# Kernel tuning notes

Measured on AMD Instinct MI355X. Metric: run time of the kernel, lower is better.

Reference implementation:

```python
import jax, jax.numpy as jnp
import numpy as np

TEMPERATURE = 1.0
CHUNK = 128  # node-block size for the curvature pass


def setup_inputs() -> dict:
    key = jax.random.key(0)
    k1, k2 = jax.random.split(key)
    N, D = 4096, 64
    x = jax.random.normal(k1, (N, D), dtype=jnp.float32)
    # sparse binary adjacency (avg degree ~16) + ring so min degree >= 2
    A = (jax.random.uniform(k2, (N, N)) < 0.004).astype(jnp.float32)
    i = jnp.arange(N)
    A = A.at[i, i].set(0.0)
    A = A.at[i, (i + 1) % N].set(1.0)
    A = A.at[(i + 1) % N, i].set(1.0)
    return {"node_embeddings": x, "adj_matrix": A}


def _physics_components(x, A):
    N, d = x.shape
    mask = A > 0
    deg = jnp.sum(A, axis=-1)                      # [N]

    # ---- total energy ----
    kinetic = jnp.sum(x * x, axis=-1)
    nb = A @ x                                     # neighbor aggregate [N,d]
    potential = -jnp.sum(x * nb, axis=-1)
    total_energy = kinetic + potential / (deg + 1e-8)

    # ---- local entropy over neighbor similarities ----
    xn = x / jnp.maximum(jnp.linalg.norm(x, axis=-1, keepdims=True), 1e-12)
    S = xn @ xn.T                                  # cosine sims [N,N]
    logits = jnp.where(mask, S / TEMPERATURE, -1e30)
    P = jax.nn.softmax(logits, axis=-1)            # masked softmax per row
    local_entropy = -jnp.sum(jnp.where(mask, P * jnp.log(P + 1e-8), 0.0), axis=-1)

    # ---- equilibrium deviation (5-NN local mean in embedding space) ----
    sq = jnp.sum(x * x, axis=-1)
    D2 = jnp.maximum(sq[:, None] + sq[None, :] - 2.0 * (x @ x.T), 1e-12)
    dist = jnp.sqrt(D2)                            # [N,N]
    _, idx = jax.lax.top_k(-dist, 6)               # smallest 6 (self first)
    local_means = jnp.mean(x[idx[:, 1:]], axis=1)  # [N,d]
    gdev = jnp.linalg.norm(x - jnp.mean(x, axis=0, keepdims=True), axis=-1)
    ldev = jnp.linalg.norm(x - local_means, axis=-1)
    equilibrium_deviation = 0.6 * gdev + 0.4 * ldev

    # ---- structural centrality ----
    en = jnp.linalg.norm(x, axis=-1)
    structural_centrality = 0.5 * deg / (N - 1) + 0.5 * en / jnp.max(en)

    # ---- information flow: unbiased var of neighbor sims ----
    ms = jnp.sum(jnp.where(mask, S, 0.0), axis=-1) / deg
    information_flow = jnp.sum(jnp.where(mask, (S - ms[:, None]) ** 2, 0.0), axis=-1) / (deg - 1.0)

    # ---- stability: 1/(1 + mean unbiased var of neighbor embeddings) ----
    m1 = nb / deg[:, None]
    ex2 = A @ (x * x)
    var_dim = (ex2 - deg[:, None] * m1 * m1) / (deg - 1.0)[:, None]
    stability = 1.0 / (1.0 + jnp.mean(var_dim, axis=-1))

    # ---- discrete curvature: 1 - mean pairwise cos angle of centered neighbors ----
    # mean_{j<k} u_j.u_k = (||sum u||^2 - sum ||u||^2) / (deg*(deg-1))
    def body(_, ids):
        xb = x[ids]                                 # [B,d]
        mb = mask[ids]                              # [B,N]
        c = x[None, :, :] - xb[:, None, :]          # [B,N,d]
        nrm = jnp.sqrt(jnp.maximum(jnp.sum(c * c, -1), 1e-12))
        u = jnp.where(mb[..., None], c / jnp.maximum(nrm, 1e-8)[..., None], 0.0)
        s = jnp.sum(u, axis=1)                      # [B,d]
        ssq = jnp.sum(u * u, axis=(1, 2))           # [B]
        db = jnp.sum(mb.astype(x.dtype), axis=-1)
        mean_cos = (jnp.sum(s * s, -1) - ssq) / (db * (db - 1.0))
        return None, 1.0 - mean_cos

    _, curv = jax.lax.scan(body, None, jnp.arange(N).reshape(-1, CHUNK))
    graph_curvature = curv.reshape(N)

    return (total_energy, local_entropy, equilibrium_deviation,
            structural_centrality, information_flow, stability, graph_curvature)


def reference(node_embeddings, adj_matrix):
    return _physics_components(node_embeddings, adj_matrix)
```

## Files before the change

### kernel.cpp

```cpp
#include <hip/hip_runtime.h>
#include <math.h>

#define NN 4096
#define DD 64
#define NSPLIT 64
#define JW 64

typedef _Float16 half8 __attribute__((ext_vector_type(8)));
typedef float f32x4 __attribute__((ext_vector_type(4)));

__device__ __forceinline__ unsigned sxu(unsigned v, int o){
  return (unsigned)__shfl_xor((int)v, o, 64);
}
__device__ __forceinline__ unsigned umn(unsigned a, unsigned b){ return a<b?a:b; }
__device__ __forceinline__ unsigned umx(unsigned a, unsigned b){ return a<b?b:a; }

__device__ __forceinline__ unsigned packkey32(float m, int j){
  float q = fmaf(m, 2048.f, 524288.f);
  q = fminf(fmaxf(q, 0.f), 1048575.f);
  return (((unsigned)q) << 12) | (unsigned)j;
}

__device__ __forceinline__ void ins5u(unsigned k, unsigned b[5]){
  bool c0=k<b[0], c1=k<b[1], c2=k<b[2], c3=k<b[3], c4=k<b[4];
  b[4] = c3 ? b[3] : (c4 ? k : b[4]);
  b[3] = c2 ? b[2] : (c3 ? k : b[3]);
  b[2] = c1 ? b[1] : (c2 ? k : b[2]);
  b[1] = c0 ? b[0] : (c1 ? k : b[1]);
  b[0] = c0 ? k : b[0];
}

__device__ __forceinline__ void mergeStage32(unsigned b[5], int st){
  unsigned p0=sxu(b[0],st),p1=sxu(b[1],st),p2=sxu(b[2],st),p3=sxu(b[3],st),p4=sxu(b[4],st);
  unsigned o0=umn(b[0],p0);
  unsigned o1=umn(umn(b[1],p1), umx(b[0],p0));
  unsigned o2=umn(umn(b[2],p2), umn(umx(b[0],p1),umx(b[1],p0)));
  unsigned o3=umn(umn(b[3],p3), umn(umx(b[0],p2), umn(umx(b[1],p1),umx(b[2],p0))));
  unsigned o4=umn(umn(b[4],p4), umn(umn(umx(b[0],p3),umx(b[1],p2)),
                                    umn(umx(b[2],p1),umx(b[3],p0))));
  b[0]=o0;b[1]=o1;b[2]=o2;b[3]=o3;b[4]=o4;
}

__device__ __forceinline__ void mergeLocal32(const unsigned a[5], const unsigned c[5], unsigned b[5]){
  b[0]=umn(a[0],c[0]);
  b[1]=umn(umn(a[1],c[1]), umx(a[0],c[0]));
  b[2]=umn(umn(a[2],c[2]), umn(umx(a[0],c[1]),umx(a[1],c[0])));
  b[3]=umn(umn(a[3],c[3]), umn(umx(a[0],c[2]), umn(umx(a[1],c[1]),umx(a[2],c[0]))));
  b[4]=umn(umn(a[4],c[4]), umn(umn(umx(a[0],c[3]),umx(a[1],c[2])),
                               umn(umx(a[2],c[1]),umx(a[3],c[0]))));
}

__global__ __launch_bounds__(256) void k_prec(const float* __restrict__ x,
                      float* __restrict__ sq,
                      _Float16* __restrict__ xh, _Float16* __restrict__ xl,
                      float* __restrict__ msum_part, float* __restrict__ maxsq_part){
  __shared__ float part[4][64];
  __shared__ float mxp[4];
  const int w = threadIdx.x>>6, lane = threadIdx.x&63;
  const int n0 = blockIdx.x*16 + w*4;
  float v0 = x[(size_t)(n0+0)*DD + lane];
  float v1 = x[(size_t)(n0+1)*DD + lane];
  float v2 = x[(size_t)(n0+2)*DD + lane];
  float v3 = x[(size_t)(n0+3)*DD + lane];
  float s0=v0*v0, s1=v1*v1, s2=v2*v2, s3=v3*v3;
#pragma unroll
  for(int o=1;o<64;o<<=1){
    s0 += __shfl_xor(s0,o,64); s1 += __shfl_xor(s1,o,64);
    s2 += __shfl_xor(s2,o,64); s3 += __shfl_xor(s3,o,64);
  }
  float vv[4] = {v0,v1,v2,v3};
  float ss[4] = {s0,s1,s2,s3};
#pragma unroll
  for(int q=0;q<4;q++){
    float v = vv[q];
    _Float16 h = (_Float16)v;
    _Float16 l = (_Float16)(v - (float)h);
    xh[(size_t)(n0+q)*DD+lane] = h;
    xl[(size_t)(n0+q)*DD+lane] = l;
    if(lane==0) sq[n0+q]=ss[q];
  }
  if(lane==0) mxp[w] = fmaxf(fmaxf(s0,s1), fmaxf(s2,s3));
  part[w][lane] = v0+v1+v2+v3; __syncthreads();
  if(w==0){
    msum_part[blockIdx.x*64 + lane] = part[0][lane]+part[1][lane]+part[2][lane]+part[3][lane];
    if(lane==0) maxsq_part[blockIdx.x] = fmaxf(fmaxf(mxp[0],mxp[1]), fmaxf(mxp[2],mxp[3]));
  }
}

__device__ __forceinline__ f32x4 gram6(const half8 J[4],
    half8 Ih0, half8 Ih1, half8 Il0, half8 Il1){
  const f32x4 z = {0.f,0.f,0.f,0.f};
  f32x4 a1 = __builtin_amdgcn_mfma_f32_16x16x32_f16(J[0], Ih0, z, 0,0,0);
  f32x4 a2 = __builtin_amdgcn_mfma_f32_16x16x32_f16(J[2], Ih0, z, 0,0,0);
  a1 = __builtin_amdgcn_mfma_f32_16x16x32_f16(J[1], Ih1, a1, 0,0,0);
  a2 = __builtin_amdgcn_mfma_f32_16x16x32_f16(J[3], Ih1, a2, 0,0,0);
  a1 = __builtin_amdgcn_mfma_f32_16x16x32_f16(J[0], Il0, a1, 0,0,0);
  a1 = __builtin_amdgcn_mfma_f32_16x16x32_f16(J[1], Il1, a1, 0,0,0);
  return a1 + a2;
}

__global__ __launch_bounds__(256, 4) void k_mega(
    const float* __restrict__ x, const float* __restrict__ A,
    const float* __restrict__ sq,
    const _Float16* __restrict__ xh, const _Float16* __restrict__ xl,
    unsigned* __restrict__ cand,
    const float* __restrict__ msum_part, const float* __restrict__ maxsq_part,
    float* __restrict__ msum, float* __restrict__ max_sq, float* __restrict__ deg_out,
    float* __restrict__ o_te, float* __restrict__ o_ent,
    float* __restrict__ o_if, float* __restrict__ o_st, float* __restrict__ o_cv)
{
  __shared__ int   nbr[4][128];
  __shared__ float Sval[4][128];
  __shared__ float rr[4][64];
  __shared__ float rm[4];
  __shared__ _Float16 jHi[512*8];
  __shared__ _Float16 jLo[512*8];
  const int bid = blockIdx.x;
  const int tid = threadIdx.x;
  const int w = tid>>6, lane = tid&63;

  if(bid == 0){
    float s = 0.f;
    for(int p=w; p<256; p+=4) s += msum_part[p*64 + lane];
    rr[w][lane] = s;
    float m = maxsq_part[w*64 + lane];
#pragma unroll
    for(int o=1;o<64;o<<=1) m = fmaxf(m, __shfl_xor(m,o,64));
    if(lane==0) rm[w] = m;
    __syncthreads();
    if(w==0){
      msum[lane] = rr[0][lane]+rr[1][lane]+rr[2][lane]+rr[3][lane];
      if(lane==0) max_sq[0] = fmaxf(fmaxf(rm[0],rm[1]), fmaxf(rm[2],rm[3]));
    }
    return;
  }

  const int t = bid - 1;
  if(t % 5 == 0){
    const int i = (t/5)*4 + w;
    const float xid = x[(size_t)i*DD + lane];
    const float sqi = sq[i];
    const float eni = sqrtf(sqi);
    const float4* A4 = (const float4*)(A + (size_t)i*NN);

    int deg = 0;
    for(int ch=0; ch<4; ++ch){
      float4 av[4];
#pragma unroll
      for(int qq=0; qq<4; ++qq) av[qq] = A4[lane + 64*(ch*4+qq)];
      int c = 0;
#pragma unroll
      for(int qq=0; qq<4; ++qq)
        c += (av[qq].x>0.f)+(av[qq].y>0.f)+(av[qq].z>0.f)+(av[qq].w>0.f);
      int sc = c;
#pragma unroll
      for(int o=1;o<64;o<<=1){ int v=__shfl_up(sc,o,64); if(lane>=o) sc+=v; }
      int off = deg + sc - c;
#pragma unroll
      for(int qq=0; qq<4; ++qq){
        int jb = 4*(lane + 64*(ch*4+qq));
        if(av[qq].x>0.f){ if(off<128) nbr[w][off]=jb+0; off++; }
        if(av[qq].y>0.f){ if(off<128) nbr[w][off]=jb+1; off++; }
        if(av[qq].z>0.f){ if(off<128) nbr[w][off]=jb+2; off++; }
        if(av[qq].w>0.f){ if(off<128) nbr[w][off]=jb+3; off++; }
      }
      deg += __shfl(sc, 63, 64);
    }

    const float degf = (float)deg;
    const int dmax = min(deg, 128);
    float nb_d=0.f, ex2_d=0.f, s_d=0.f, ssq=0.f;

    for(int c0=0; c0<dmax; c0+=8){
      int jq[8]; float aq[8], qq[8];
#pragma unroll
      for(int q=0;q<8;q++) jq[q] = nbr[w][min(c0+q, dmax-1)];
#pragma unroll
      for(int q=0;q<8;q++) aq[q] = x[(size_t)jq[q]*DD + lane];
#pragma unroll
      for(int q=0;q<8;q++) qq[q] = sq[jq[q]];
      asm volatile("" :: "v"(aq[0]), "v"(aq[1]), "v"(aq[2]), "v"(aq[3]),
                         "v"(aq[4]), "v"(aq[5]), "v"(aq[6]), "v"(aq[7]));
      float p[8];
#pragma unroll
      for(int q=0;q<8;q++) p[q] = xid*aq[q];
#pragma unroll
      for(int o=1;o<64;o<<=1){
#pragma unroll
        for(int q=0;q<8;q++) p[q] += __shfl_xor(p[q],o,64);
      }
#pragma unroll
      for(int q=0;q<8;q++){
        const bool valid = (c0+q) < deg;
        float c2 = fmaxf(sqi + qq[q] - 2.0f*p[q], 1e-12f);
        float inv = 1.0f/fmaxf(sqrtf(c2), 1e-8f);
        nb_d  += valid ? aq[q] : 0.f;
        ex2_d += valid ? aq[q]*aq[q] : 0.f;
        s_d   += valid ? (aq[q]-xid)*inv : 0.f;
        ssq   += valid ? c2*inv*inv : 0.f;
        if(valid && lane==q) Sval[w][c0+q] = p[q]/(eni*sqrtf(qq[q]));
      }
    }

    float t0 = xid*nb_d;
    float m1 = nb_d/degf;
    float t1 = (ex2_d - degf*m1*m1)/(degf-1.0f);
    float t2 = s_d*s_d;
    float t3 = 0.f, t4 = 0.f;
    for(int s=lane; s<dmax; s+=64){ float v=Sval[w][s]; t3 += expf(v); t4 += v; }
#pragma unroll
    for(int o=1;o<64;o<<=1){
      t0 += __shfl_xor(t0,o,64); t1 += __shfl_xor(t1,o,64); t2 += __shfl_xor(t2,o,64);
      t3 += __shfl_xor(t3,o,64); t4 += __shfl_xor(t4,o,64);
    }
    const float pot = t0, varm = t1*(1.0f/DD), s2 = t2, se = t3, ms = t4/degf;

    float e0=0.f, e1=0.f;
    const float inv_se = 1.0f/se;
    for(int s=lane; s<dmax; s+=64){
      float v = Sval[w][s];
      float pp = expf(v)*inv_se;
      e0 -= pp*logf(pp + 1e-8f);
      float dv = v-ms; e1 += dv*dv;
    }
#pragma unroll
    for(int o=1;o<64;o<<=1){ e0 += __shfl_xor(e0,o,64); e1 += __shfl_xor(e1,o,64); }

    if(lane==0){
      o_te[i]  = sqi - pot/(degf + 1e-8f);
      o_ent[i] = e0;
      o_if[i]  = e1/(degf-1.0f);
      o_st[i]  = 1.0f/(1.0f + varm);
      o_cv[i]  = 1.0f - (s2 - ssq)/(degf*(degf-1.0f));
      deg_out[i] = degf;
    }
  } else {
    const int kid = (t/5)*4 + (t%5) - 1;
    const int split = kid & (NSPLIT-1);
    const int strip = (kid >> 6)*4 + w;
    const int ibase = strip*16, j0 = split*JW;
    const int col = lane & 15, kg = lane >> 4;
    const int vo = col*DD + kg*8;
    const int myi = ibase + col;

#pragma unroll
    for(int q=0;q<2;q++){
      int g = q*256 + tid;
      int r = g >> 3;
      int c = (g & 7) ^ (r & 7);
      const _Float16* srcH = xh + (size_t)(j0 + r)*DD + c*8;
      const _Float16* srcL = xl + (size_t)(j0 + r)*DD + c*8;
      __builtin_amdgcn_global_load_lds(
        (const __attribute__((address_space(1))) unsigned int*)srcH,
        (__attribute__((address_space(3))) unsigned int*)(jHi + g*8), 16, 0, 0);
      __builtin_amdgcn_global_load_lds(
        (const __attribute__((address_space(1))) unsigned int*)srcL,
        (__attribute__((address_space(3))) unsigned int*)(jLo + g*8), 16, 0, 0);
    }

    const _Float16* pih = xh + (size_t)ibase*DD + vo;
    const _Float16* pil = xl + (size_t)ibase*DD + vo;
    const half8 Ih0 = *(const half8*)(pih);
    const half8 Ih1 = *(const half8*)(pih+32);
    const half8 Il0 = *(const half8*)(pil);
    const half8 Il1 = *(const half8*)(pil+32);

    const int jb0 = j0 + kg*4;
    float4 sq0 = *(const float4*)(sq + jb0);
    float4 sq1 = *(const float4*)(sq + jb0 + 16);
    float4 sq2 = *(const float4*)(sq + jb0 + 32);
    float4 sq3 = *(const float4*)(sq + jb0 + 48);

    __syncthreads();

    half8 JT[4][4];
#pragma unroll
    for(int tt=0; tt<4; tt++){
      const int rl = tt*16 + col;
      const int sw = rl & 7;
      JT[tt][0] = *(const half8*)(jHi + (rl*8 + ( kg      ^ sw))*8);
      JT[tt][1] = *(const half8*)(jHi + (rl*8 + ((kg + 4) ^ sw))*8);
      JT[tt][2] = *(const half8*)(jLo + (rl*8 + ( kg      ^ sw))*8);
      JT[tt][3] = *(const half8*)(jLo + (rl*8 + ((kg + 4) ^ sw))*8);
    }

    f32x4 d0 = gram6(JT[0], Ih0, Ih1, Il0, Il1);
    f32x4 d1 = gram6(JT[1], Ih0, Ih1, Il0, Il1);
    f32x4 d2 = gram6(JT[2], Ih0, Ih1, Il0, Il1);
    f32x4 d3 = gram6(JT[3], Ih0, Ih1, Il0, Il1);

    unsigned bA[5], bB[5];
#pragma unroll
    for(int k=0;k<5;k++){ bA[k]=0xFFFFFFFFu; bB[k]=0xFFFFFFFFu; }

    {
      float s0v[4]={sq0.x,sq0.y,sq0.z,sq0.w};
      float s2v[4]={sq2.x,sq2.y,sq2.z,sq2.w};
#pragma unroll
      for(int r=0;r<4;r++){
        unsigned k0 = packkey32(fmaf(-2.0f, d0[r], s0v[r]), jb0+r);
        k0 = (jb0+r==myi) ? 0xFFFFFFFFu : k0;
        ins5u(k0, bA);
        unsigned k2 = packkey32(fmaf(-2.0f, d2[r], s2v[r]), jb0+32+r);
        k2 = (jb0+32+r==myi) ? 0xFFFFFFFFu : k2;
        ins5u(k2, bA);
      }
    }
    {
      float s1v[4]={sq1.x,sq1.y,sq1.z,sq1.w};
      float s3v[4]={sq3.x,sq3.y,sq3.z,sq3.w};
#pragma unroll
      for(int r=0;r<4;r++){
        unsigned k1 = packkey32(fmaf(-2.0f, d1[r], s1v[r]), jb0+16+r);
        k1 = (jb0+16+r==myi) ? 0xFFFFFFFFu : k1;
        ins5u(k1, bB);
        unsigned k3 = packkey32(fmaf(-2.0f, d3[r], s3v[r]), jb0+48+r);
        k3 = (jb0+48+r==myi) ? 0xFFFFFFFFu : k3;
        ins5u(k3, bB);
      }
    }

    unsigned b[5];
    mergeLocal32(bA, bB, b);
    mergeStage32(b, 16);
    mergeStage32(b, 32);

    if(kg==0){
#pragma unroll
      for(int k=0;k<5;k++)
        cand[((size_t)myi*NSPLIT + split)*5 + k] = b[k];
    }
  }
}

__global__ __launch_bounds__(256) void k_nnsel(
    const float* __restrict__ x, const unsigned* __restrict__ cand,
    const float* __restrict__ msum, const float* __restrict__ max_sq,
    const float* __restrict__ deg, const float* __restrict__ sq,
    float* __restrict__ o_eq, float* __restrict__ o_sc)
{
  const int w = threadIdx.x>>6, l = threadIdx.x&63;
  const int i = blockIdx.x*4 + w;
  const unsigned* cr = cand + (size_t)i*(NSPLIT*5);
  unsigned c0 = cr[l], c1 = cr[64+l], c2 = cr[128+l], c3 = cr[192+l], c4 = cr[256+l];

  int sel[5];
#pragma unroll
  for(int k=0;k<5;k++){
    unsigned d = umn(umn(umn(c0,c1),umn(c2,c3)),c4);
#pragma unroll
    for(int o=1;o<64;o<<=1) d = umn(d, sxu(d,o));
    sel[k] = (int)(d & 0xFFFu);
    if(c0==d) c0=0xFFFFFFFFu;
    else if(c1==d) c1=0xFFFFFFFFu;
    else if(c2==d) c2=0xFFFFFFFFu;
    else if(c3==d) c3=0xFFFFFFFFu;
    else if(c4==d) c4=0xFFFFFFFFu;
  }

  float smv=0.f;
#pragma unroll
  for(int k=0;k<5;k++) smv += x[(size_t)sel[k]*DD + l];
  float xiv = x[(size_t)i*DD + l];
  float lv = xiv - smv*0.2f;
  float gv = xiv - msum[l]*(1.0f/NN);
  float pl = lv*lv, pg = gv*gv;
#pragma unroll
  for(int o=1;o<64;o<<=1){ pl += __shfl_xor(pl,o,64); pg += __shfl_xor(pg,o,64); }
  if(l==0){
    o_eq[i] = 0.6f*sqrtf(pg) + 0.4f*sqrtf(pl);
    o_sc[i] = 0.5f*deg[i]/(float)(NN-1) + 0.5f*sqrtf(sq[i])/sqrtf(max_sq[0]);
  }
}

extern "C" void kernel_launch(void* const* d_in, const int* in_sizes, int n_in,
                              void* d_out, int out_size, void* d_ws, size_t ws_size,
                              hipStream_t stream) {
  const float* x = (const float*)d_in[0];
  const float* A = (const float*)d_in[1];
  float* out = (float*)d_out;
  float* ws  = (float*)d_ws;
  float*     sq        = ws;
  float*     msum      = ws + 4096;
  float*     max_sq    = ws + 4160;
  float*     deg       = ws + 4224;
  float*     msum_part = ws + 8320;
  float*     maxsq_part= ws + 24704;
  _Float16*  xh        = (_Float16*)(ws + 24960);
  _Float16*  xl        = (_Float16*)(ws + 156032);
  unsigned*  cand      = (unsigned*)(ws + 287104);

  k_prec<<<NN/16, 256, 0, stream>>>(x, sq, xh, xl, msum_part, maxsq_part);
  k_mega<<<5*NN/4 + 1, 256, 0, stream>>>(x, A, sq, xh, xl, cand,
                                         msum_part, maxsq_part, msum, max_sq, deg,
                                         out, out+NN, out+4*NN, out+5*NN, out+6*NN);
  k_nnsel<<<NN/4, 256, 0, stream>>>(x, cand, msum, max_sq, deg, sq,
                                    out+2*NN, out+3*NN);
}
```

Baseline: 58.81 us.

## Widen KNN column tiles to 256 with double-buffered LDS staging, fewer splits

Each KNN block now covers 256 candidate columns in four 64-column chunks instead of one chunk. It double-buffers the fp16 hi/lo tiles in LDS so the next chunk's async global-to-LDS load overlaps the current chunk's MFMA and top-5 insertion. With 16 splits instead of 64, the grid interleaves row-stat blocks and KNN blocks 1:1 and writes a quarter as many candidates, which simplifies the final selection merge. The cost is fewer, longer blocks, twice the LDS tile footprint, and a sync per chunk.

```diff
diff --git a/kernel.cpp b/kernel.cpp
--- a/kernel.cpp
+++ b/kernel.cpp
@@ -3,8 +3,8 @@
 
 #define NN 4096
 #define DD 64
-#define NSPLIT 64
-#define JW 64
+#define NSPLIT 16
+#define JW 256
 
 typedef _Float16 half8 __attribute__((ext_vector_type(8)));
 typedef float f32x4 __attribute__((ext_vector_type(4)));
@@ -113,8 +113,8 @@
   __shared__ float Sval[4][128];
   __shared__ float rr[4][64];
   __shared__ float rm[4];
-  __shared__ _Float16 jHi[512*8];
-  __shared__ _Float16 jLo[512*8];
+  __shared__ _Float16 jHi[2][512*8];
+  __shared__ _Float16 jLo[2][512*8];
   const int bid = blockIdx.x;
   const int tid = threadIdx.x;
   const int w = tid>>6, lane = tid&63;
@@ -136,8 +136,8 @@
   }
 
   const int t = bid - 1;
-  if(t % 5 == 0){
-    const int i = (t/5)*4 + w;
+  if((t & 1) == 0){
+    const int i = (t>>1)*4 + w;
     const float xid = x[(size_t)i*DD + lane];
     const float sqi = sq[i];
     const float eni = sqrtf(sqi);
@@ -235,28 +235,31 @@
       deg_out[i] = degf;
     }
   } else {
-    const int kid = (t/5)*4 + (t%5) - 1;
+    const int kid = t >> 1;
     const int split = kid & (NSPLIT-1);
-    const int strip = (kid >> 6)*4 + w;
+    const int strip = (kid >> 4)*4 + w;
     const int ibase = strip*16, j0 = split*JW;
     const int col = lane & 15, kg = lane >> 4;
     const int vo = col*DD + kg*8;
     const int myi = ibase + col;
 
-#pragma unroll
-    for(int q=0;q<2;q++){
-      int g = q*256 + tid;
-      int r = g >> 3;
-      int c = (g & 7) ^ (r & 7);
-      const _Float16* srcH = xh + (size_t)(j0 + r)*DD + c*8;
-      const _Float16* srcL = xl + (size_t)(j0 + r)*DD + c*8;
-      __builtin_amdgcn_global_load_lds(
-        (const __attribute__((address_space(1))) unsigned int*)srcH,
-        (__attribute__((address_space(3))) unsigned int*)(jHi + g*8), 16, 0, 0);
-      __builtin_amdgcn_global_load_lds(
-        (const __attribute__((address_space(1))) unsigned int*)srcL,
-        (__attribute__((address_space(3))) unsigned int*)(jLo + g*8), 16, 0, 0);
-    }
+#define STAGE(BUF, CH) { \
+    _Pragma("unroll") \
+    for(int q_=0;q_<2;q_++){ \
+      int g_ = q_*256 + tid; \
+      int r_ = g_ >> 3; \
+      int c_ = (g_ & 7) ^ (r_ & 7); \
+      const _Float16* sH_ = xh + (size_t)(j0 + (CH)*64 + r_)*DD + c_*8; \
+      const _Float16* sL_ = xl + (size_t)(j0 + (CH)*64 + r_)*DD + c_*8; \
+      __builtin_amdgcn_global_load_lds( \
+        (const __attribute__((address_space(1))) unsigned int*)sH_, \
+        (__attribute__((address_space(3))) unsigned int*)(jHi[BUF] + g_*8), 16, 0, 0); \
+      __builtin_amdgcn_global_load_lds( \
+        (const __attribute__((address_space(1))) unsigned int*)sL_, \
+        (__attribute__((address_space(3))) unsigned int*)(jLo[BUF] + g_*8), 16, 0, 0); \
+    } }
+
+    STAGE(0, 0);
 
     const _Float16* pih = xh + (size_t)ibase*DD + vo;
     const _Float16* pil = xl + (size_t)ibase*DD + vo;
@@ -265,60 +268,47 @@
     const half8 Il0 = *(const half8*)(pil);
     const half8 Il1 = *(const half8*)(pil+32);
 
-    const int jb0 = j0 + kg*4;
-    float4 sq0 = *(const float4*)(sq + jb0);
-    float4 sq1 = *(const float4*)(sq + jb0 + 16);
-    float4 sq2 = *(const float4*)(sq + jb0 + 32);
-    float4 sq3 = *(const float4*)(sq + jb0 + 48);
-
-    __syncthreads();
-
-    half8 JT[4][4];
-#pragma unroll
-    for(int tt=0; tt<4; tt++){
-      const int rl = tt*16 + col;
-      const int sw = rl & 7;
-      JT[tt][0] = *(const half8*)(jHi + (rl*8 + ( kg      ^ sw))*8);
-      JT[tt][1] = *(const half8*)(jHi + (rl*8 + ((kg + 4) ^ sw))*8);
-      JT[tt][2] = *(const half8*)(jLo + (rl*8 + ( kg      ^ sw))*8);
-      JT[tt][3] = *(const half8*)(jLo + (rl*8 + ((kg + 4) ^ sw))*8);
-    }
-
-    f32x4 d0 = gram6(JT[0], Ih0, Ih1, Il0, Il1);
-    f32x4 d1 = gram6(JT[1], Ih0, Ih1, Il0, Il1);
-    f32x4 d2 = gram6(JT[2], Ih0, Ih1, Il0, Il1);
-    f32x4 d3 = gram6(JT[3], Ih0, Ih1, Il0, Il1);
-
     unsigned bA[5], bB[5];
 #pragma unroll
     for(int k=0;k<5;k++){ bA[k]=0xFFFFFFFFu; bB[k]=0xFFFFFFFFu; }
 
-    {
-      float s0v[4]={sq0.x,sq0.y,sq0.z,sq0.w};
-      float s2v[4]={sq2.x,sq2.y,sq2.z,sq2.w};
-#pragma unroll
-      for(int r=0;r<4;r++){
-        unsigned k0 = packkey32(fmaf(-2.0f, d0[r], s0v[r]), jb0+r);
-        k0 = (jb0+r==myi) ? 0xFFFFFFFFu : k0;
-        ins5u(k0, bA);
-        unsigned k2 = packkey32(fmaf(-2.0f, d2[r], s2v[r]), jb0+32+r);
-        k2 = (jb0+32+r==myi) ? 0xFFFFFFFFu : k2;
-        ins5u(k2, bA);
-      }
-    }
-    {
-      float s1v[4]={sq1.x,sq1.y,sq1.z,sq1.w};
-      float s3v[4]={sq3.x,sq3.y,sq3.z,sq3.w};
-#pragma unroll
-      for(int r=0;r<4;r++){
-        unsigned k1 = packkey32(fmaf(-2.0f, d1[r], s1v[r]), jb0+16+r);
-        k1 = (jb0+16+r==myi) ? 0xFFFFFFFFu : k1;
-        ins5u(k1, bB);
-        unsigned k3 = packkey32(fmaf(-2.0f, d3[r], s3v[r]), jb0+48+r);
-        k3 = (jb0+48+r==myi) ? 0xFFFFFFFFu : k3;
-        ins5u(k3, bB);
-      }
-    }
+#pragma unroll
+    for(int ch=0; ch<4; ch++){
+      __syncthreads();
+      if(ch<3) STAGE((ch+1)&1, ch+1);
+      const _Float16* bh = jHi[ch&1];
+      const _Float16* bl = jLo[ch&1];
+      const int jb0 = j0 + ch*64 + kg*4;
+      float4 sq0 = *(const float4*)(sq + jb0);
+      float4 sq1 = *(const float4*)(sq + jb0 + 16);
+      float4 sq2 = *(const float4*)(sq + jb0 + 32);
+      float4 sq3 = *(const float4*)(sq + jb0 + 48);
+
+      half8 JT[4];
+#define TILE(TT, SQV, LIST) { \
+      const int rl_ = (TT)*16 + col; \
+      const int sw_ = rl_ & 7; \
+      JT[0] = *(const half8*)(bh + (rl_*8 + ( kg      ^ sw_))*8); \
+      JT[1] = *(const half8*)(bh + (rl_*8 + ((kg + 4) ^ sw_))*8); \
+      JT[2] = *(const half8*)(bl + (rl_*8 + ( kg      ^ sw_))*8); \
+      JT[3] = *(const half8*)(bl + (rl_*8 + ((kg + 4) ^ sw_))*8); \
+      f32x4 d_ = gram6(JT, Ih0, Ih1, Il0, Il1); \
+      float sv_[4] = {SQV.x, SQV.y, SQV.z, SQV.w}; \
+      const int jt0_ = jb0 + (TT)*16; \
+      _Pragma("unroll") \
+      for(int r_=0;r_<4;r_++){ \
+        unsigned kk_ = packkey32(fmaf(-2.0f, d_[r_], sv_[r_]), jt0_+r_); \
+        kk_ = (jt0_+r_==myi) ? 0xFFFFFFFFu : kk_; \
+        ins5u(kk_, LIST); \
+      } }
+
+      TILE(0, sq0, bA);
+      TILE(1, sq1, bB);
+      TILE(2, sq2, bA);
+      TILE(3, sq3, bB);
+#undef TILE
+    }
+#undef STAGE
 
     unsigned b[5];
     mergeLocal32(bA, bB, b);
@@ -342,20 +332,18 @@
   const int w = threadIdx.x>>6, l = threadIdx.x&63;
   const int i = blockIdx.x*4 + w;
   const unsigned* cr = cand + (size_t)i*(NSPLIT*5);
-  unsigned c0 = cr[l], c1 = cr[64+l], c2 = cr[128+l], c3 = cr[192+l], c4 = cr[256+l];
+  unsigned c0 = cr[l];
+  unsigned c1 = (l < 16) ? cr[64+l] : 0xFFFFFFFFu;
 
   int sel[5];
 #pragma unroll
   for(int k=0;k<5;k++){
-    unsigned d = umn(umn(umn(c0,c1),umn(c2,c3)),c4);
+    unsigned d = umn(c0,c1);
 #pragma unroll
     for(int o=1;o<64;o<<=1) d = umn(d, sxu(d,o));
     sel[k] = (int)(d & 0xFFFu);
     if(c0==d) c0=0xFFFFFFFFu;
     else if(c1==d) c1=0xFFFFFFFFu;
-    else if(c2==d) c2=0xFFFFFFFFu;
-    else if(c3==d) c3=0xFFFFFFFFu;
-    else if(c4==d) c4=0xFFFFFFFFu;
   }
 
   float smv=0.f;
@@ -391,9 +379,9 @@
   unsigned*  cand      = (unsigned*)(ws + 287104);
 
   k_prec<<<NN/16, 256, 0, stream>>>(x, sq, xh, xl, msum_part, maxsq_part);
-  k_mega<<<5*NN/4 + 1, 256, 0, stream>>>(x, A, sq, xh, xl, cand,
-                                         msum_part, maxsq_part, msum, max_sq, deg,
-                                         out, out+NN, out+4*NN, out+5*NN, out+6*NN);
+  k_mega<<<NN/2 + 1, 256, 0, stream>>>(x, A, sq, xh, xl, cand,
+                                       msum_part, maxsq_part, msum, max_sq, deg,
+                                       out, out+NN, out+4*NN, out+5*NN, out+6*NN);
   k_nnsel<<<NN/4, 256, 0, stream>>>(x, cand, msum, max_sq, deg, sq,
                                     out+2*NN, out+3*NN);
 }
```

Result: faster. 56.97 us (-3.1%).
